# Kernel optimization log

Measured on AMD Instinct MI355X. Metric: run time of the kernel, lower is better.

The kernel has to match this reference:

```python
import jax, jax.numpy as jnp
import numpy as np

N = 3072
E = 32 * N
H = 8
IN_F = 64
OUT_F = 16
ALPHA = 0.2  # LeakyReLU slope
NEG_INF = -9e15


def setup_inputs() -> dict:
    key = jax.random.key(0)
    k1, k2, k3, k4, k5 = jax.random.split(key, 5)
    h = jax.random.normal(k1, (N, IN_F), dtype=jnp.float32)
    edge_index = jax.random.randint(k2, (2, E), 0, N, dtype=jnp.int64)
    S = jax.random.uniform(k3, (N, N), dtype=jnp.float32)
    W = jax.random.normal(k4, (H, IN_F, OUT_F), dtype=jnp.float32) * 0.2
    a = jax.random.normal(k5, (H, 2 * OUT_F, 1), dtype=jnp.float32) * 0.3
    raw_gamma = jnp.ones((H,), dtype=jnp.float32)
    return {"h": h, "edge_index": edge_index, "S": S, "W": W, "a": a, "raw_gamma": raw_gamma}


def reference(h, edge_index, S, W, a, raw_gamma):
    n = h.shape[0]
    # dense adjacency from edge list (to_dense_adj semantics: adj[src, dst] += 1)
    adj = jnp.zeros((n, n), dtype=h.dtype).at[edge_index[0], edge_index[1]].add(1.0)
    # per-head projection: Wh [H, N, O]
    Wh = jnp.einsum('nf,hfo->hno', h, W)
    o = W.shape[2]
    a1 = a[:, :o, 0]  # [H, O]
    a2 = a[:, o:, 0]  # [H, O]
    e1 = jnp.einsum('hno,ho->hn', Wh, a1)  # Wh @ a[:O]
    e2 = jnp.einsum('hno,ho->hn', Wh, a2)  # Wh @ a[O:]
    e = jax.nn.leaky_relu(e1[:, :, None] + e2[:, None, :], ALPHA)  # [H, N, N]
    att = jnp.where(adj[None] > 0, e, jnp.asarray(NEG_INF, e.dtype))
    gamma = jax.nn.softplus(raw_gamma)  # [H], non-negative gate
    att = att * (1.0 + gamma[:, None, None] * S[None])
    att = jax.nn.softmax(att, axis=-1)  # row softmax (dim=1 of [N, N])
    # dropout is identity in eval mode
    h_prime = jnp.einsum('hnm,hmo->hno', att, Wh)  # [H, N, O]
    h_prime = jax.nn.elu(h_prime)  # concat=True per head
    # concat heads along feature dim -> [N, H*O]
    return jnp.transpose(h_prime, (1, 0, 2)).reshape(n, -1)
```

## Files before the change

kernel.cpp:

```cpp
#include <hip/hip_runtime.h>
#include <math.h>

#define N_NODES 3072
#define H_HEADS 8
#define IN_FEAT 64
#define OUT_FEAT 16
#define WORDS_PER_ROW 96
#define MAXD 96
#define SCATTER_BLOCKS 384
#define WH_NPB 16
#define WH_BLOCKS (N_NODES / WH_NPB)

__launch_bounds__(256)
__global__ void scatter_and_wh_kernel(const int* __restrict__ ei, int E,
                                      unsigned int* __restrict__ bits,
                                      const float* __restrict__ hfeat,
                                      const float* __restrict__ W,
                                      const float* __restrict__ a,
                                      float* __restrict__ Wh,
                                      float* __restrict__ e1t,
                                      float* __restrict__ e2t) {
    __shared__ __align__(16) float Wt[H_HEADS][OUT_FEAT][68];
    __shared__ __align__(16) float hs[WH_NPB][IN_FEAT];

    int tid = threadIdx.x;
    if (blockIdx.x < SCATTER_BLOCKS) {
        int e = blockIdx.x * 256 + tid;
        if (e < E) {
            int r = ei[e];
            int c = ei[E + e];
            atomicOr(&bits[r * WORDS_PER_ROW + (c >> 5)], 1u << (c & 31));
        }
        return;
    }

    int node_base = (blockIdx.x - SCATTER_BLOCKS) * WH_NPB;
    for (int idx = tid; idx < H_HEADS * IN_FEAT * OUT_FEAT; idx += 256) {
        int hh = idx >> 10, f = (idx >> 4) & 63, o = idx & 15;
        Wt[hh][o][f] = W[idx];
    }
    for (int idx = tid; idx < WH_NPB * IN_FEAT; idx += 256)
        hs[idx >> 6][idx & 63] = hfeat[node_base * IN_FEAT + idx];
    __syncthreads();

    int ng = tid >> 7;
    int hh = (tid >> 4) & 7;
    int o  = tid & 15;
    float a1v = a[hh * 2 * OUT_FEAT + o];
    float a2v = a[hh * 2 * OUT_FEAT + OUT_FEAT + o];

    float4 w[16];
#pragma unroll
    for (int q = 0; q < 16; ++q)
        w[q] = *(const float4*)&Wt[hh][o][4 * q];

    for (int n = ng; n < WH_NPB; n += 2) {
        float acc = 0.f;
#pragma unroll
        for (int q = 0; q < 16; ++q) {
            float4 hv = *(const float4*)&hs[n][4 * q];
            acc = fmaf(hv.x, w[q].x, acc);
            acc = fmaf(hv.y, w[q].y, acc);
            acc = fmaf(hv.z, w[q].z, acc);
            acc = fmaf(hv.w, w[q].w, acc);
        }
        int node = node_base + n;
        Wh[(hh * N_NODES + node) * OUT_FEAT + o] = acc;
        float p1 = acc * a1v, p2 = acc * a2v;
#pragma unroll
        for (int m = 1; m < 16; m <<= 1) {
            p1 += __shfl_xor(p1, m, 64);
            p2 += __shfl_xor(p2, m, 64);
        }
        if (o == 0) {
            e1t[node * H_HEADS + hh] = p1;
            e2t[node * H_HEADS + hh] = p2;
        }
    }
}

__launch_bounds__(256)
__global__ void gat_main_kernel(const unsigned int* __restrict__ bits,
                                const float* __restrict__ S,
                                const float* __restrict__ Wh,
                                const float* __restrict__ e1t,
                                const float* __restrict__ e2t,
                                const float* __restrict__ raw_gamma,
                                float* __restrict__ out) {
    __shared__ int lds_j[MAXD];
    __shared__ float lds_s[MAXD];
    __shared__ float lds_e2h[H_HEADS][MAXD];
    __shared__ float lds_p[H_HEADS][MAXD];
    __shared__ int lds_cnt;
    __shared__ int fb_j;
    int i = blockIdx.x;
    int tid = threadIdx.x;
    int wave = tid >> 6, lane = tid & 63;

    if (wave == 0) {
        unsigned int w0 = bits[i * WORDS_PER_ROW + lane];
        unsigned int w1 = (lane < WORDS_PER_ROW - 64)
                              ? bits[i * WORDS_PER_ROW + 64 + lane] : 0u;
        int c = __popc(w0) + __popc(w1);
        int s = c;
#pragma unroll
        for (int d = 1; d < 64; d <<= 1) {
            int v = __shfl_up(s, d, 64);
            if (lane >= d) s += v;
        }
        int off = s - c;
        if (lane == 63) lds_cnt = s;
        unsigned int b = w0;
        int base = lane << 5;
        while (b) {
            int bit = __ffs(b) - 1; b &= b - 1;
            if (off < MAXD) lds_j[off] = base + bit;
            ++off;
        }
        b = w1; base = (64 + lane) << 5;
        while (b) {
            int bit = __ffs(b) - 1; b &= b - 1;
            if (off < MAXD) lds_j[off] = base + bit;
            ++off;
        }
    }
    __syncthreads();
    int cnt = lds_cnt;
    if (cnt > MAXD) cnt = MAXD;

    if (tid < cnt) {
        int j = lds_j[tid];
        lds_s[tid] = S[i * N_NODES + j];
        const float4* ep = (const float4*)&e2t[j * H_HEADS];
        float4 ea = ep[0], eb = ep[1];
        lds_e2h[0][tid] = ea.x; lds_e2h[1][tid] = ea.y;
        lds_e2h[2][tid] = ea.z; lds_e2h[3][tid] = ea.w;
        lds_e2h[4][tid] = eb.x; lds_e2h[5][tid] = eb.y;
        lds_e2h[6][tid] = eb.z; lds_e2h[7][tid] = eb.w;
    }
    __syncthreads();

    if (cnt == 0) {
        if (wave == 0) {
            float bm = 3.4e38f; int bj = 0;
            for (int j = lane; j < N_NODES; j += 64) {
                float sv = S[i * N_NODES + j];
                if (sv < bm) { bm = sv; bj = j; }
            }
            for (int m = 1; m < 64; m <<= 1) {
                float bm2 = __shfl_xor(bm, m, 64);
                int bj2 = __shfl_xor(bj, m, 64);
                if (bm2 < bm || (bm2 == bm && bj2 < bj)) { bm = bm2; bj = bj2; }
            }
            if (lane == 0) fb_j = bj;
        }
        __syncthreads();
        int jj = fb_j;
        if (tid < H_HEADS * OUT_FEAT) {
            int h2 = tid >> 4, o2 = tid & 15;
            float x = Wh[(h2 * N_NODES + jj) * OUT_FEAT + o2];
            out[i * (H_HEADS * OUT_FEAT) + h2 * OUT_FEAT + o2] =
                x > 0.f ? x : __expf(x) - 1.f;
        }
        return;
    }

    int half = lane >> 5;
    int hl = lane & 31;
    int hh = wave * 2 + half;
    float g = log1pf(__expf(raw_gamma[hh]));
    float e1v = e1t[i * H_HEADS + hh];
    float l = 0.f;
    for (int k = hl; k < cnt; k += 32) {
        float x = e1v + lds_e2h[hh][k];
        x = x > 0.f ? x : 0.2f * x;
        float p = __expf(x * (1.f + g * lds_s[k]));
        lds_p[hh][k] = p;
        l += p;
    }
#pragma unroll
    for (int m = 1; m < 32; m <<= 1)
        l += __shfl_xor(l, m, 64);

    int kgrp = hl >> 4, o = hl & 15;
    float acc = 0.f;
    for (int kk = kgrp; kk < cnt; kk += 2)
        acc = fmaf(lds_p[hh][kk], Wh[(hh * N_NODES + lds_j[kk]) * OUT_FEAT + o], acc);
    acc += __shfl_xor(acc, 16, 64);
    if (kgrp == 0) {
        float x = acc / l;
        out[i * (H_HEADS * OUT_FEAT) + hh * OUT_FEAT + o] =
            x > 0.f ? x : __expf(x) - 1.f;
    }
}

extern "C" void kernel_launch(void* const* d_in, const int* in_sizes, int n_in,
                              void* d_out, int out_size, void* d_ws, size_t ws_size,
                              hipStream_t stream) {
    const float* hfeat = (const float*)d_in[0];
    const int* ei      = (const int*)d_in[1];
    const float* S     = (const float*)d_in[2];
    const float* W     = (const float*)d_in[3];
    const float* a     = (const float*)d_in[4];
    const float* rg    = (const float*)d_in[5];
    float* out = (float*)d_out;

    char* ws = (char*)d_ws;
    unsigned int* bits = (unsigned int*)ws;
    float* Wh = (float*)(ws + 1179648);
    float* e1t = (float*)(ws + 1179648 + 1572864);
    float* e2t = e1t + N_NODES * H_HEADS;

    hipMemsetAsync(bits, 0, (size_t)N_NODES * WORDS_PER_ROW * 4, stream);

    int E = in_sizes[1] / 2;
    scatter_and_wh_kernel<<<SCATTER_BLOCKS + WH_BLOCKS, 256, 0, stream>>>(
        ei, E, bits, hfeat, W, a, Wh, e1t, e2t);

    gat_main_kernel<<<N_NODES, 256, 0, stream>>>(bits, S, Wh, e1t, e2t, rg, out);
}
```

Measured before the change: 111.8 us.

## Vectorize edge scatter, parallelize bitmap compaction across waves, float4 Wh gather

```diff
diff --git a/kernel.cpp b/kernel.cpp
--- a/kernel.cpp
+++ b/kernel.cpp
@@ -7,8 +7,8 @@
 #define OUT_FEAT 16
 #define WORDS_PER_ROW 96
 #define MAXD 96
-#define SCATTER_BLOCKS 384
-#define WH_NPB 16
+#define EDGES_PER_THREAD 4
+#define WH_NPB 32
 #define WH_BLOCKS (N_NODES / WH_NPB)
 
 __launch_bounds__(256)
@@ -24,17 +24,27 @@
     __shared__ __align__(16) float hs[WH_NPB][IN_FEAT];
 
     int tid = threadIdx.x;
-    if (blockIdx.x < SCATTER_BLOCKS) {
-        int e = blockIdx.x * 256 + tid;
-        if (e < E) {
-            int r = ei[e];
-            int c = ei[E + e];
-            atomicOr(&bits[r * WORDS_PER_ROW + (c >> 5)], 1u << (c & 31));
+    int sb = (E + 256 * EDGES_PER_THREAD - 1) / (256 * EDGES_PER_THREAD);
+    if (blockIdx.x < sb) {
+        int e0 = (blockIdx.x * 256 + tid) * EDGES_PER_THREAD;
+        if (((E & 3) == 0) && (e0 + 3 < E)) {
+            int4 r4 = *(const int4*)&ei[e0];
+            int4 c4 = *(const int4*)&ei[E + e0];
+            atomicOr(&bits[r4.x * WORDS_PER_ROW + (c4.x >> 5)], 1u << (c4.x & 31));
+            atomicOr(&bits[r4.y * WORDS_PER_ROW + (c4.y >> 5)], 1u << (c4.y & 31));
+            atomicOr(&bits[r4.z * WORDS_PER_ROW + (c4.z >> 5)], 1u << (c4.z & 31));
+            atomicOr(&bits[r4.w * WORDS_PER_ROW + (c4.w >> 5)], 1u << (c4.w & 31));
+        } else {
+            for (int e = e0; e < E && e < e0 + EDGES_PER_THREAD; ++e) {
+                int r = ei[e];
+                int c = ei[E + e];
+                atomicOr(&bits[r * WORDS_PER_ROW + (c >> 5)], 1u << (c & 31));
+            }
         }
         return;
     }
 
-    int node_base = (blockIdx.x - SCATTER_BLOCKS) * WH_NPB;
+    int node_base = (blockIdx.x - sb) * WH_NPB;
     for (int idx = tid; idx < H_HEADS * IN_FEAT * OUT_FEAT; idx += 256) {
         int hh = idx >> 10, f = (idx >> 4) & 63, o = idx & 15;
         Wt[hh][o][f] = W[idx];
@@ -91,41 +101,40 @@
     __shared__ float lds_s[MAXD];
     __shared__ float lds_e2h[H_HEADS][MAXD];
     __shared__ float lds_p[H_HEADS][MAXD];
-    __shared__ int lds_cnt;
+    __shared__ int lds_wtot[4];
     __shared__ int fb_j;
     int i = blockIdx.x;
     int tid = threadIdx.x;
     int wave = tid >> 6, lane = tid & 63;
 
-    if (wave == 0) {
-        unsigned int w0 = bits[i * WORDS_PER_ROW + lane];
-        unsigned int w1 = (lane < WORDS_PER_ROW - 64)
-                              ? bits[i * WORDS_PER_ROW + 64 + lane] : 0u;
-        int c = __popc(w0) + __popc(w1);
-        int s = c;
-#pragma unroll
-        for (int d = 1; d < 64; d <<= 1) {
-            int v = __shfl_up(s, d, 64);
-            if (lane >= d) s += v;
-        }
-        int off = s - c;
-        if (lane == 63) lds_cnt = s;
+    unsigned int w0 = 0u;
+    if (lane < 24) w0 = bits[i * WORDS_PER_ROW + wave * 24 + lane];
+    int c = __popc(w0);
+    int s = c;
+#pragma unroll
+    for (int d = 1; d < 32; d <<= 1) {
+        int v = __shfl_up(s, d, 64);
+        if (lane >= d) s += v;
+    }
+    int wtot = __shfl(s, 23, 64);
+    if (lane == 0) lds_wtot[wave] = wtot;
+    __syncthreads();
+    int base = 0;
+#pragma unroll
+    for (int k = 0; k < 4; ++k)
+        if (k < wave) base += lds_wtot[k];
+    int cnt = lds_wtot[0] + lds_wtot[1] + lds_wtot[2] + lds_wtot[3];
+    {
+        int off = base + s - c;
         unsigned int b = w0;
-        int base = lane << 5;
+        int nbase = (wave * 24 + lane) << 5;
         while (b) {
             int bit = __ffs(b) - 1; b &= b - 1;
-            if (off < MAXD) lds_j[off] = base + bit;
+            if (off < MAXD) lds_j[off] = nbase + bit;
             ++off;
         }
-        b = w1; base = (64 + lane) << 5;
-        while (b) {
-            int bit = __ffs(b) - 1; b &= b - 1;
-            if (off < MAXD) lds_j[off] = base + bit;
-            ++off;
-        }
-    }
-    __syncthreads();
-    int cnt = lds_cnt;
+    }
+    __syncthreads();
     if (cnt > MAXD) cnt = MAXD;
 
     if (tid < cnt) {
@@ -182,15 +191,34 @@
     for (int m = 1; m < 32; m <<= 1)
         l += __shfl_xor(l, m, 64);
 
-    int kgrp = hl >> 4, o = hl & 15;
-    float acc = 0.f;
-    for (int kk = kgrp; kk < cnt; kk += 2)
-        acc = fmaf(lds_p[hh][kk], Wh[(hh * N_NODES + lds_j[kk]) * OUT_FEAT + o], acc);
-    acc += __shfl_xor(acc, 16, 64);
+    int kgrp = hl >> 2;
+    int q = hl & 3;
+    float4 facc = make_float4(0.f, 0.f, 0.f, 0.f);
+    for (int kk = kgrp; kk < cnt; kk += 8) {
+        float p = lds_p[hh][kk];
+        float4 wv = *(const float4*)&Wh[((hh * N_NODES + lds_j[kk]) << 4) + (q << 2)];
+        facc.x = fmaf(p, wv.x, facc.x);
+        facc.y = fmaf(p, wv.y, facc.y);
+        facc.z = fmaf(p, wv.z, facc.z);
+        facc.w = fmaf(p, wv.w, facc.w);
+    }
+#pragma unroll
+    for (int m = 4; m < 32; m <<= 1) {
+        facc.x += __shfl_xor(facc.x, m, 64);
+        facc.y += __shfl_xor(facc.y, m, 64);
+        facc.z += __shfl_xor(facc.z, m, 64);
+        facc.w += __shfl_xor(facc.w, m, 64);
+    }
     if (kgrp == 0) {
-        float x = acc / l;
-        out[i * (H_HEADS * OUT_FEAT) + hh * OUT_FEAT + o] =
-            x > 0.f ? x : __expf(x) - 1.f;
+        float4 x;
+        x.x = facc.x / l; x.y = facc.y / l;
+        x.z = facc.z / l; x.w = facc.w / l;
+        float4 o4;
+        o4.x = x.x > 0.f ? x.x : __expf(x.x) - 1.f;
+        o4.y = x.y > 0.f ? x.y : __expf(x.y) - 1.f;
+        o4.z = x.z > 0.f ? x.z : __expf(x.z) - 1.f;
+        o4.w = x.w > 0.f ? x.w : __expf(x.w) - 1.f;
+        *(float4*)&out[i * (H_HEADS * OUT_FEAT) + hh * OUT_FEAT + (q << 2)] = o4;
     }
 }
 
@@ -214,7 +242,8 @@
     hipMemsetAsync(bits, 0, (size_t)N_NODES * WORDS_PER_ROW * 4, stream);
 
     int E = in_sizes[1] / 2;
-    scatter_and_wh_kernel<<<SCATTER_BLOCKS + WH_BLOCKS, 256, 0, stream>>>(
+    int sb = (E + 256 * EDGES_PER_THREAD - 1) / (256 * EDGES_PER_THREAD);
+    scatter_and_wh_kernel<<<sb + WH_BLOCKS, 256, 0, stream>>>(
         ei, E, bits, hfeat, W, a, Wh, e1t, e2t);
 
     gat_main_kernel<<<N_NODES, 256, 0, stream>>>(bits, S, Wh, e1t, e2t, rg, out);
```

Result: faster. 108.6 us (-2.8%).
